# Optimization experiments

Measured on AMD Instinct MI355X. Metric: run time of the kernel, lower is better.

The kernel has to match this reference:

```python
import jax, jax.numpy as jnp
import numpy as np

NH, K = 16, 4  # num_heads, num_points


def _ln(x, g, b):
    m = x.mean(-1, keepdims=True)
    v = jnp.var(x, axis=-1, keepdims=True)
    return (x - m) / jnp.sqrt(v + 1e-5) * g + b


def setup_inputs() -> dict:
    key = jax.random.key(0)
    ks = jax.random.split(key, 12)
    B, S, D = 16, 1024, 1024
    HD = D // NH
    def lin(k, fi, fo, scale=1.0):
        return jax.random.normal(k, (fi, fo), jnp.float32) * (scale / np.sqrt(fi))
    z = lambda n: jnp.zeros((n,), jnp.float32)
    return {
        "source": jax.random.normal(ks[0], (B, S, D), jnp.float32),
        "target": jax.random.normal(ks[1], (B, S, D), jnp.float32),
        "Wq": lin(ks[2], D, D), "bq": z(D),
        "Wo1": lin(ks[3], HD, 64), "bo1": z(64),
        "Wo2": lin(ks[4], 64, 2 * K, 0.1), "bo2": z(2 * K),
        "Wa": lin(ks[5], HD, K), "ba": z(K),
        "Wv": lin(ks[6], D, D), "bv": z(D),
        "Wout": lin(ks[7], D, D), "bout": z(D),
        "gq": jnp.ones((D,), jnp.float32), "bq_ln": z(D),
        "gkv": jnp.ones((D,), jnp.float32), "bkv_ln": z(D),
        "gffn": jnp.ones((D,), jnp.float32), "bffn_ln": z(D),
        "W1": lin(ks[8], D, 4 * D), "b1": z(4 * D),
        "W2": lin(ks[9], 4 * D, D), "b2": z(D),
    }


def _forward(source, target, Wq, bq, Wo1, bo1, Wo2, bo2, Wa, ba, Wv, bv,
             Wout, bout, gq, bq_ln, gkv, bkv_ln, gffn, bffn_ln, W1, b1, W2, b2):
    B, S, D = source.shape
    HD = D // NH
    Hs = int(round(S ** 0.5)); Ws = Hs  # S = H*W square grid

    q_norm = _ln(source, gq, bq_ln)
    v_norm = _ln(target, gkv, bkv_ln)
    q = (q_norm @ Wq + bq).reshape(B, S, NH, HD)
    # value map per head: (B, NH, H, W, HD)
    v = (v_norm @ Wv + bv).reshape(B, Hs, Ws, NH, HD).transpose(0, 3, 1, 2, 4)
    v_flat = v.reshape(B, NH, Hs * Ws, HD)

    # learned offsets: tanh(MLP(q)) * 0.5, in normalized [-1,1] coords
    h = jax.nn.relu(q @ Wo1 + bo1)
    off = jnp.tanh((h @ Wo2 + bo2).reshape(B, S, NH, K, 2)) * 0.5

    # reference grid: ref_grid[i*W+j] = (ref_x[j], ref_y[i])
    rx = jnp.linspace(-1.0, 1.0, Ws)
    ry = jnp.linspace(-1.0, 1.0, Hs)
    gx, gy = jnp.meshgrid(rx, ry)  # 'xy' indexing
    ref = jnp.stack([gx, gy], -1).reshape(S, 2)
    pts = ref[None, :, None, None, :] + off  # (B, S, NH, K, 2), last dim = (x, y)

    # grid_sample, bilinear, align_corners=True, padding_mode='zeros'
    x = (pts[..., 0] + 1.0) * 0.5 * (Ws - 1)
    y = (pts[..., 1] + 1.0) * 0.5 * (Hs - 1)
    x = jnp.moveaxis(x, 1, 2)  # (B, NH, S, K)
    y = jnp.moveaxis(y, 1, 2)
    x0 = jnp.floor(x); y0 = jnp.floor(y)
    wx1 = x - x0; wy1 = y - y0
    x0i = x0.astype(jnp.int32); y0i = y0.astype(jnp.int32)

    def gather(xi, yi, w):
        m = (xi >= 0) & (xi <= Ws - 1) & (yi >= 0) & (yi <= Hs - 1)
        idx = jnp.clip(yi, 0, Hs - 1) * Ws + jnp.clip(xi, 0, Ws - 1)
        g = jnp.take_along_axis(v_flat, idx.reshape(B, NH, S * K, 1), axis=2)
        return g.reshape(B, NH, S, K, HD) * (w * m)[..., None]

    sampled = (gather(x0i, y0i, (1.0 - wx1) * (1.0 - wy1))
               + gather(x0i + 1, y0i, wx1 * (1.0 - wy1))
               + gather(x0i, y0i + 1, (1.0 - wx1) * wy1)
               + gather(x0i + 1, y0i + 1, wx1 * wy1))  # (B, NH, S, K, HD)

    attn = jax.nn.softmax(q @ Wa + ba, axis=-1)  # (B, S, NH, K)
    head_out = jnp.einsum('bsnk,bnskd->bsnd', attn, sampled).reshape(B, S, D)

    src = source + (head_out @ Wout + bout)
    f = jax.nn.gelu(_ln(src, gffn, bffn_ln) @ W1 + b1, approximate=False)
    return src + (f @ W2 + b2)


def reference(source, target, Wq, bq, Wo1, bo1, Wo2, bo2, Wa, ba, Wv, bv,
              Wout, bout, gq, bq_ln, gkv, bkv_ln, gffn, bffn_ln, W1, b1, W2, b2):
    return _forward(source, target, Wq, bq, Wo1, bo1, Wo2, bo2, Wa, ba, Wv, bv,
                    Wout, bout, gq, bq_ln, gkv, bkv_ln, gffn, bffn_ln, W1, b1, W2, b2)
```

## Files before the change

### kernel.cpp

```cpp
#include <hip/hip_runtime.h>

typedef __attribute__((ext_vector_type(8))) short short8;
typedef __attribute__((ext_vector_type(4))) float f32x4;

#define DEV __device__ __forceinline__

DEV float bf2f(unsigned short u) { return __uint_as_float(((unsigned)u) << 16); }
DEV unsigned short f2bf(float f) {
  unsigned u = __float_as_uint(f);
  u += 0x7FFF + ((u >> 16) & 1);
  return (unsigned short)(u >> 16);
}

#define GLOAD_LDS16(gptr, lptr)                                                              \
  __builtin_amdgcn_global_load_lds((const __attribute__((address_space(1))) void*)(gptr),   \
                                   (__attribute__((address_space(3))) void*)(lptr), 16, 0, 0)

__global__ __launch_bounds__(256) void wt_transpose_bf16(const float* __restrict__ W,
                                                         unsigned short* __restrict__ Wt,
                                                         int K, int N) {
  __shared__ float t[32][33];
  int k0 = blockIdx.x * 32, n0 = blockIdx.y * 32;
  int tx = threadIdx.x, ty = threadIdx.y;
#pragma unroll
  for (int i = 0; i < 4; ++i)
    t[ty + 8 * i][tx] = W[(long)(k0 + ty + 8 * i) * N + n0 + tx];
  __syncthreads();
#pragma unroll
  for (int i = 0; i < 4; ++i)
    Wt[(long)(n0 + ty + 8 * i) * K + k0 + tx] = f2bf(t[tx][ty + 8 * i]);
}

__global__ __launch_bounds__(256) void ln_to_bf16(const float* __restrict__ x,
                                                  const float* __restrict__ g,
                                                  const float* __restrict__ b,
                                                  unsigned short* __restrict__ y) {
  const long row = blockIdx.x;
  const int tid = threadIdx.x;
  float4 v = *(const float4*)(x + row * 1024 + tid * 4);
  float s = v.x + v.y + v.z + v.w;
  float s2 = v.x * v.x + v.y * v.y + v.z * v.z + v.w * v.w;
#pragma unroll
  for (int o = 32; o > 0; o >>= 1) { s += __shfl_down(s, o); s2 += __shfl_down(s2, o); }
  __shared__ float red[8];
  __shared__ float mv[2];
  int wv = tid >> 6, ln = tid & 63;
  if (ln == 0) { red[wv] = s; red[4 + wv] = s2; }
  __syncthreads();
  if (tid == 0) {
    float a = red[0] + red[1] + red[2] + red[3];
    float q = red[4] + red[5] + red[6] + red[7];
    float mean = a * (1.f / 1024.f);
    mv[0] = mean;
    mv[1] = rsqrtf(q * (1.f / 1024.f) - mean * mean + 1e-5f);
  }
  __syncthreads();
  float mean = mv[0], rstd = mv[1];
  float4 gg = *(const float4*)(g + tid * 4);
  float4 bb = *(const float4*)(b + tid * 4);
  ushort4 o;
  o.x = f2bf((v.x - mean) * rstd * gg.x + bb.x);
  o.y = f2bf((v.y - mean) * rstd * gg.y + bb.y);
  o.z = f2bf((v.z - mean) * rstd * gg.z + bb.z);
  o.w = f2bf((v.w - mean) * rstd * gg.w + bb.w);
  *(ushort4*)(y + row * 1024 + tid * 4) = o;
}

template <int EPI>
__global__ __launch_bounds__(512, 2) void gemm_bf16(const unsigned short* __restrict__ A,
                                                    const unsigned short* __restrict__ Bt,
                                                    const float* __restrict__ bias,
                                                    const float* __restrict__ res,
                                                    void* __restrict__ out,
                                                    int N, int K, int ldb) {
  __shared__ __align__(16) char smem[131072];
  const int tid = threadIdx.x;
  const int wave = tid >> 6, lane = tid & 63;
  const int wm = wave >> 2, wn = wave & 3;
  const long row0 = (long)blockIdx.x * 256;
  const long col0 = (long)blockIdx.y * 256;
  const int NT = K >> 5;

  f32x4 acc[8][4];
#pragma unroll
  for (int i = 0; i < 8; ++i)
#pragma unroll
    for (int n = 0; n < 4; ++n) acc[i][n] = f32x4{0.f, 0.f, 0.f, 0.f};

  const int srow = wave * 16 + (lane >> 2);
  const int kc_ph = lane & 3;

  auto STAGE = [&](const unsigned short* base, long ld, long r0, int U, char* dst16k) {
#pragma unroll
    for (int j = 0; j < 2; ++j) {
      const int row = j * 128 + srow;
      const int kc = kc_ph ^ ((row >> 1) & 3);
      GLOAD_LDS16(base + (r0 + row) * ld + U * 32 + kc * 8, dst16k + j * 8192 + wave * 1024);
    }
  };
  auto RD = [&](const char* sb, int row) -> short8 {
    const int kc = (lane >> 4) ^ ((row >> 1) & 3);
    return *(const short8*)(sb + row * 64 + kc * 16);
  };

#pragma unroll
  for (int U = 0; U < 3; ++U) {
    STAGE(A, K, row0, U, smem + U * 32768);
    STAGE(Bt, ldb, col0, U, smem + U * 32768 + 16384);
  }
  asm volatile("s_waitcnt vmcnt(8)" ::: "memory");
  __builtin_amdgcn_s_barrier();

  for (int T = 0; T < NT; ++T) {
    const char* sA = smem + (T & 3) * 32768;
    const char* sB = sA + 16384;
    char* stslot = smem + ((T + 3) & 3) * 32768;
    const bool do_stage = (T + 3 < NT);

    short8 af[4], bf[4];
#pragma unroll
    for (int i = 0; i < 4; ++i) af[i] = RD(sA, wm * 128 + i * 16 + (lane & 15));
#pragma unroll
    for (int n = 0; n < 4; ++n) bf[n] = RD(sB, wn * 64 + n * 16 + (lane & 15));
    if (do_stage) STAGE(A, K, row0, T + 3, stslot);
    __builtin_amdgcn_s_barrier();
    __builtin_amdgcn_s_setprio(1);
#pragma unroll
    for (int i = 0; i < 4; ++i)
#pragma unroll
      for (int n = 0; n < 4; ++n)
        acc[i][n] = __builtin_amdgcn_mfma_f32_16x16x32_bf16(af[i], bf[n], acc[i][n], 0, 0, 0);
    __builtin_amdgcn_s_setprio(0);
    __builtin_amdgcn_s_barrier();

#pragma unroll
    for (int i = 0; i < 4; ++i) af[i] = RD(sA, wm * 128 + 64 + i * 16 + (lane & 15));
    if (do_stage) STAGE(Bt, ldb, col0, T + 3, stslot + 16384);
    if (T < NT - 3) {
      asm volatile("s_waitcnt vmcnt(8)" ::: "memory");
    } else if (T == NT - 3) {
      asm volatile("s_waitcnt vmcnt(4)" ::: "memory");
    } else if (T == NT - 2) {
      asm volatile("s_waitcnt vmcnt(0)" ::: "memory");
    }
    __builtin_amdgcn_s_barrier();
    __builtin_amdgcn_s_setprio(1);
#pragma unroll
    for (int i = 0; i < 4; ++i)
#pragma unroll
      for (int n = 0; n < 4; ++n)
        acc[4 + i][n] =
            __builtin_amdgcn_mfma_f32_16x16x32_bf16(af[i], bf[n], acc[4 + i][n], 0, 0, 0);
    __builtin_amdgcn_s_setprio(0);
    __builtin_amdgcn_s_barrier();
  }

  const int lr = lane >> 4, lc = lane & 15;
#pragma unroll
  for (int i = 0; i < 8; ++i) {
#pragma unroll
    for (int n = 0; n < 4; ++n) {
      const long gcol = col0 + wn * 64 + n * 16 + lc;
      const float bvv = (EPI == 5) ? 0.f : bias[gcol];
#pragma unroll
      for (int r = 0; r < 4; ++r) {
        const long grow = row0 + wm * 128 + i * 16 + lr * 4 + r;
        float val = acc[i][n][r] + bvv;
        if (EPI == 0) {
          ((float*)out)[grow * N + gcol] = val;
        } else if (EPI == 1) {
          const int b_ = (int)(grow >> 10), hw = (int)(grow & 1023);
          const int nh = (int)(gcol >> 6), hd = (int)(gcol & 63);
          ((unsigned short*)out)[((long)(b_ * 16 + nh) << 16) + hw * 64 + hd] = f2bf(val);
        } else if (EPI == 2) {
          ((float*)out)[grow * N + gcol] = val + res[grow * N + gcol];
        } else if (EPI == 3) {
          float gl = 0.5f * val * (1.f + erff(val * 0.70710678118654752f));
          ((unsigned short*)out)[grow * N + gcol] = f2bf(gl);
        } else {
          ((float*)out)[grow * N + gcol] = val + res[grow * N + gcol];
        }
      }
    }
  }
}

__global__ __launch_bounds__(256) void offset_attn_mlp(
    const float* __restrict__ qf,
    const float* __restrict__ Wo1, const float* __restrict__ bo1,
    const float* __restrict__ Wo2, const float* __restrict__ bo2,
    const float* __restrict__ Wa, const float* __restrict__ ba,
    float* __restrict__ coords) {
  const int r = blockIdx.x * 256 + threadIdx.x;
  const int s = (r >> 4) & 1023;

  float qr[64];
  const float* qp = qf + (long)r * 64;
#pragma unroll
  for (int i = 0; i < 16; ++i) *(float4*)(qr + 4 * i) = *(const float4*)(qp + 4 * i);

  float off[8];
#pragma unroll
  for (int o = 0; o < 8; ++o) off[o] = bo2[o];

#pragma unroll 1
  for (int jj = 0; jj < 8; ++jj) {
    float hacc[8];
#pragma unroll
    for (int o = 0; o < 8; ++o) hacc[o] = bo1[jj * 8 + o];
#pragma unroll
    for (int i = 0; i < 64; ++i) {
      const float qv = qr[i];
#pragma unroll
      for (int o = 0; o < 8; ++o) hacc[o] = fmaf(qv, Wo1[i * 64 + jj * 8 + o], hacc[o]);
    }
#pragma unroll
    for (int jo = 0; jo < 8; ++jo) {
      const float hj = fmaxf(hacc[jo], 0.f);
      const int j = jj * 8 + jo;
#pragma unroll
      for (int o = 0; o < 8; ++o) off[o] = fmaf(hj, Wo2[j * 8 + o], off[o]);
    }
  }

  float lg[4];
#pragma unroll
  for (int k = 0; k < 4; ++k) lg[k] = ba[k];
#pragma unroll
  for (int i = 0; i < 64; ++i) {
    const float qv = qr[i];
#pragma unroll
    for (int k = 0; k < 4; ++k) lg[k] = fmaf(qv, Wa[i * 4 + k], lg[k]);
  }
  const float mx = fmaxf(fmaxf(lg[0], lg[1]), fmaxf(lg[2], lg[3]));
  const float e0 = expf(lg[0] - mx), e1 = expf(lg[1] - mx), e2 = expf(lg[2] - mx),
              e3 = expf(lg[3] - mx);
  const float inv = 1.f / (e0 + e1 + e2 + e3);

  const float sx = (float)(s & 31), sy = (float)(s >> 5);
  float4 xv, yv, av;
  xv.x = sx + tanhf(off[0]) * 7.75f; yv.x = sy + tanhf(off[1]) * 7.75f;
  xv.y = sx + tanhf(off[2]) * 7.75f; yv.y = sy + tanhf(off[3]) * 7.75f;
  xv.z = sx + tanhf(off[4]) * 7.75f; yv.z = sy + tanhf(off[5]) * 7.75f;
  xv.w = sx + tanhf(off[6]) * 7.75f; yv.w = sy + tanhf(off[7]) * 7.75f;
  av.x = e0 * inv; av.y = e1 * inv; av.z = e2 * inv; av.w = e3 * inv;
  float* cp = coords + (long)r * 16;
  *(float4*)(cp + 0) = xv;
  *(float4*)(cp + 4) = yv;
  *(float4*)(cp + 8) = av;
}

__global__ __launch_bounds__(256) void deform_gather(
    const unsigned short* __restrict__ v_flat, const float* __restrict__ coords,
    unsigned short* __restrict__ head_out) {
  const int tid = threadIdx.x, wave = tid >> 6, lane = tid & 63;
  const int m = blockIdx.x * 4 + wave;
  const int b = m >> 14, nh = (m >> 10) & 15, s = m & 1023;
  const long r = (long)(b * 1024 + s) * 16 + nh;

  float cf = 0.f;
  if (lane < 12) cf = coords[r * 16 + lane];
  const unsigned short* vb = v_flat + ((long)(b * 16 + nh) << 16);

  float o = 0.f;
#pragma unroll
  for (int k = 0; k < 4; ++k) {
    const float xp = __shfl(cf, k), yp = __shfl(cf, 4 + k), ak = __shfl(cf, 8 + k);
    const float x0f = floorf(xp), y0f = floorf(yp);
    const int x0 = (int)x0f, y0 = (int)y0f;
    const float wx1 = xp - x0f, wy1 = yp - y0f;
    const float wx0 = 1.f - wx1, wy0 = 1.f - wy1;
    float smp = 0.f;
#pragma unroll
    for (int cn = 0; cn < 4; ++cn) {
      const int xi = x0 + (cn & 1), yi = y0 + (cn >> 1);
      const float w = (cn & 1 ? wx1 : wx0) * (cn >> 1 ? wy1 : wy0);
      const bool msk = (xi >= 0) & (xi <= 31) & (yi >= 0) & (yi <= 31);
      const int xc = min(max(xi, 0), 31), yc = min(max(yi, 0), 31);
      const float vv = bf2f(vb[(yc * 32 + xc) * 64 + lane]);
      smp = fmaf(vv, msk ? w : 0.f, smp);
    }
    o = fmaf(ak, smp, o);
  }
  head_out[r * 64 + lane] = f2bf(o);
}

extern "C" void kernel_launch(void* const* d_in, const int* in_sizes, int n_in,
                              void* d_out, int out_size, void* d_ws, size_t ws_size,
                              hipStream_t stream) {
  const float* source = (const float*)d_in[0];
  const float* target = (const float*)d_in[1];
  const float* Wq = (const float*)d_in[2];
  const float* bq = (const float*)d_in[3];
  const float* Wo1 = (const float*)d_in[4];
  const float* bo1 = (const float*)d_in[5];
  const float* Wo2 = (const float*)d_in[6];
  const float* bo2 = (const float*)d_in[7];
  const float* Wa = (const float*)d_in[8];
  const float* ba = (const float*)d_in[9];
  const float* Wv = (const float*)d_in[10];
  const float* bv = (const float*)d_in[11];
  const float* Wout = (const float*)d_in[12];
  const float* bout = (const float*)d_in[13];
  const float* gq = (const float*)d_in[14];
  const float* bq_ln = (const float*)d_in[15];
  const float* gkv = (const float*)d_in[16];
  const float* bkv_ln = (const float*)d_in[17];
  const float* gffn = (const float*)d_in[18];
  const float* bffn_ln = (const float*)d_in[19];
  const float* W1 = (const float*)d_in[20];
  const float* b1 = (const float*)d_in[21];
  const float* W2 = (const float*)d_in[22];
  const float* b2 = (const float*)d_in[23];

  char* ws = (char*)d_ws;
  const size_t MB = 1u << 20;
  if (ws_size < 150 * MB) return;

  unsigned short* q_norm = (unsigned short*)(ws + 0);
  unsigned short* v_flat = (unsigned short*)(ws + 0);
  unsigned short* v_norm = (unsigned short*)(ws + 32 * MB);
  float* coords = (float*)(ws + 32 * MB);
  unsigned short* ffn_in = (unsigned short*)(ws + 32 * MB);
  float* qf = (float*)(ws + 64 * MB);
  unsigned short* head_out = (unsigned short*)(ws + 64 * MB);
  unsigned short* f_buf = (unsigned short*)(ws + 64 * MB);
  unsigned short* Wq_t = (unsigned short*)(ws + 128 * MB);
  unsigned short* Wv_t = (unsigned short*)(ws + 130 * MB);
  unsigned short* Wout_t = (unsigned short*)(ws + 132 * MB);
  unsigned short* W1_t = (unsigned short*)(ws + 134 * MB);
  unsigned short* W2_t = (unsigned short*)(ws + 142 * MB);
  float* src = (float*)d_out;

  dim3 tb(32, 8);
  wt_transpose_bf16<<<dim3(32, 32), tb, 0, stream>>>(Wq, Wq_t, 1024, 1024);
  wt_transpose_bf16<<<dim3(32, 32), tb, 0, stream>>>(Wv, Wv_t, 1024, 1024);
  wt_transpose_bf16<<<dim3(32, 32), tb, 0, stream>>>(Wout, Wout_t, 1024, 1024);
  wt_transpose_bf16<<<dim3(32, 128), tb, 0, stream>>>(W1, W1_t, 1024, 4096);
  wt_transpose_bf16<<<dim3(128, 32), tb, 0, stream>>>(W2, W2_t, 4096, 1024);

  ln_to_bf16<<<16384, 256, 0, stream>>>(source, gq, bq_ln, q_norm);
  ln_to_bf16<<<16384, 256, 0, stream>>>(target, gkv, bkv_ln, v_norm);

  gemm_bf16<0><<<dim3(64, 4), 512, 0, stream>>>(q_norm, Wq_t, bq, nullptr, qf, 1024, 1024, 1024);
  gemm_bf16<1><<<dim3(64, 4), 512, 0, stream>>>(v_norm, Wv_t, bv, nullptr, v_flat, 1024, 1024, 1024);

  offset_attn_mlp<<<1024, 256, 0, stream>>>(qf, Wo1, bo1, Wo2, bo2, Wa, ba, coords);
  deform_gather<<<65536, 256, 0, stream>>>(v_flat, coords, head_out);

  gemm_bf16<2><<<dim3(64, 4), 512, 0, stream>>>(head_out, Wout_t, bout, source, src, 1024, 1024, 1024);

  ln_to_bf16<<<16384, 256, 0, stream>>>(src, gffn, bffn_ln, ffn_in);

  gemm_bf16<3><<<dim3(64, 8), 512, 0, stream>>>(ffn_in, W1_t, b1, nullptr, f_buf, 2048, 1024, 1024);
  gemm_bf16<2><<<dim3(64, 4), 512, 0, stream>>>(f_buf, W2_t, b2, src, src, 1024, 2048, 4096);
  gemm_bf16<3><<<dim3(64, 8), 512, 0, stream>>>(ffn_in, W1_t + (long)2048 * 1024, b1 + 2048,
                                                nullptr, f_buf, 2048, 1024, 1024);
  gemm_bf16<5><<<dim3(64, 4), 512, 0, stream>>>(f_buf, W2_t + 2048, nullptr, src, src, 1024, 2048, 4096);
}
```

Measured before the change: 873.2 us.

## Replace deep-pipelined 256x256 GEMM with simple 128x128 tile kernel for most GEMMs

The general GEMM now uses 128x128 tiles with 256 threads, a 64-wide K step, an XOR-swizzled 32KB LDS buffer and a full wait plus barrier every iteration, in place of the 4-stage pipelined 256x256 design. A copy of the old deep-pipelined kernel, renamed gemm_deep_gelu, is kept for the first W1 half and now issues its LDS-direct loads through inline asm that sets m0. The goal is more blocks and better occupancy and wave coverage across CUs. The cost is losing load/compute overlap and reading each operand more times from global memory in the simpler kernel.

```diff
diff --git a/kernel.cpp b/kernel.cpp
--- a/kernel.cpp
+++ b/kernel.cpp
@@ -15,6 +15,12 @@
 #define GLOAD_LDS16(gptr, lptr)                                                              \
   __builtin_amdgcn_global_load_lds((const __attribute__((address_space(1))) void*)(gptr),   \
                                    (__attribute__((address_space(3))) void*)(lptr), 16, 0, 0)
+
+DEV void stage16_asm(const void* gaddr, unsigned lds_off_sgpr) {
+  asm volatile("s_mov_b32 m0, %1\n\t"
+               "global_load_lds_dwordx4 %0, off"
+               :: "v"(gaddr), "s"(lds_off_sgpr) : "memory");
+}
 
 __global__ __launch_bounds__(256) void wt_transpose_bf16(const float* __restrict__ W,
                                                          unsigned short* __restrict__ Wt,
@@ -67,105 +73,70 @@
 }
 
 template <int EPI>
-__global__ __launch_bounds__(512, 2) void gemm_bf16(const unsigned short* __restrict__ A,
-                                                    const unsigned short* __restrict__ Bt,
-                                                    const float* __restrict__ bias,
-                                                    const float* __restrict__ res,
-                                                    void* __restrict__ out,
-                                                    int N, int K, int ldb) {
-  __shared__ __align__(16) char smem[131072];
+__global__ __launch_bounds__(256) void gemm_bf16(const unsigned short* __restrict__ A,
+                                                 const unsigned short* __restrict__ Bt,
+                                                 const float* __restrict__ bias,
+                                                 const float* __restrict__ res,
+                                                 void* __restrict__ out,
+                                                 int N, int K, int ldb) {
+  __shared__ __align__(16) char smem[32768];
   const int tid = threadIdx.x;
   const int wave = tid >> 6, lane = tid & 63;
-  const int wm = wave >> 2, wn = wave & 3;
-  const long row0 = (long)blockIdx.x * 256;
-  const long col0 = (long)blockIdx.y * 256;
-  const int NT = K >> 5;
-
-  f32x4 acc[8][4];
-#pragma unroll
-  for (int i = 0; i < 8; ++i)
-#pragma unroll
-    for (int n = 0; n < 4; ++n) acc[i][n] = f32x4{0.f, 0.f, 0.f, 0.f};
-
-  const int srow = wave * 16 + (lane >> 2);
-  const int kc_ph = lane & 3;
-
-  auto STAGE = [&](const unsigned short* base, long ld, long r0, int U, char* dst16k) {
-#pragma unroll
-    for (int j = 0; j < 2; ++j) {
-      const int row = j * 128 + srow;
-      const int kc = kc_ph ^ ((row >> 1) & 3);
-      GLOAD_LDS16(base + (r0 + row) * ld + U * 32 + kc * 8, dst16k + j * 8192 + wave * 1024);
-    }
-  };
-  auto RD = [&](const char* sb, int row) -> short8 {
-    const int kc = (lane >> 4) ^ ((row >> 1) & 3);
-    return *(const short8*)(sb + row * 64 + kc * 16);
-  };
-
-#pragma unroll
-  for (int U = 0; U < 3; ++U) {
-    STAGE(A, K, row0, U, smem + U * 32768);
-    STAGE(Bt, ldb, col0, U, smem + U * 32768 + 16384);
-  }
-  asm volatile("s_waitcnt vmcnt(8)" ::: "memory");
-  __builtin_amdgcn_s_barrier();
-
-  for (int T = 0; T < NT; ++T) {
-    const char* sA = smem + (T & 3) * 32768;
-    const char* sB = sA + 16384;
-    char* stslot = smem + ((T + 3) & 3) * 32768;
-    const bool do_stage = (T + 3 < NT);
-
-    short8 af[4], bf[4];
-#pragma unroll
-    for (int i = 0; i < 4; ++i) af[i] = RD(sA, wm * 128 + i * 16 + (lane & 15));
-#pragma unroll
-    for (int n = 0; n < 4; ++n) bf[n] = RD(sB, wn * 64 + n * 16 + (lane & 15));
-    if (do_stage) STAGE(A, K, row0, T + 3, stslot);
-    __builtin_amdgcn_s_barrier();
-    __builtin_amdgcn_s_setprio(1);
-#pragma unroll
-    for (int i = 0; i < 4; ++i)
-#pragma unroll
-      for (int n = 0; n < 4; ++n)
-        acc[i][n] = __builtin_amdgcn_mfma_f32_16x16x32_bf16(af[i], bf[n], acc[i][n], 0, 0, 0);
-    __builtin_amdgcn_s_setprio(0);
-    __builtin_amdgcn_s_barrier();
-
-#pragma unroll
-    for (int i = 0; i < 4; ++i) af[i] = RD(sA, wm * 128 + 64 + i * 16 + (lane & 15));
-    if (do_stage) STAGE(Bt, ldb, col0, T + 3, stslot + 16384);
-    if (T < NT - 3) {
-      asm volatile("s_waitcnt vmcnt(8)" ::: "memory");
-    } else if (T == NT - 3) {
-      asm volatile("s_waitcnt vmcnt(4)" ::: "memory");
-    } else if (T == NT - 2) {
-      asm volatile("s_waitcnt vmcnt(0)" ::: "memory");
-    }
-    __builtin_amdgcn_s_barrier();
-    __builtin_amdgcn_s_setprio(1);
-#pragma unroll
-    for (int i = 0; i < 4; ++i)
-#pragma unroll
-      for (int n = 0; n < 4; ++n)
-        acc[4 + i][n] =
-            __builtin_amdgcn_mfma_f32_16x16x32_bf16(af[i], bf[n], acc[4 + i][n], 0, 0, 0);
-    __builtin_amdgcn_s_setprio(0);
-    __builtin_amdgcn_s_barrier();
+  const int wm = wave >> 1, wn = wave & 1;
+  const long row0 = (long)blockIdx.x * 128;
+  const long col0 = (long)blockIdx.y * 128;
+
+  f32x4 acc[4][4];
+#pragma unroll
+  for (int i = 0; i < 4; ++i)
+#pragma unroll
+    for (int j = 0; j < 4; ++j) acc[i][j] = f32x4{0.f, 0.f, 0.f, 0.f};
+
+  const int gg = lane & 7;
+  const int rsub = lane >> 3;
+
+  for (int kt = 0; kt < K; kt += 64) {
+#pragma unroll
+    for (int i = 0; i < 4; ++i) {
+      const int c = wave * 4 + i;
+      const int r = c * 8 + rsub;
+      const int kg = gg ^ rsub;
+      GLOAD_LDS16(A + (row0 + r) * (long)K + kt + kg * 8, smem + c * 1024);
+      GLOAD_LDS16(Bt + (col0 + r) * (long)ldb + kt + kg * 8, smem + 16384 + c * 1024);
+    }
+    asm volatile("s_waitcnt vmcnt(0)" ::: "memory");
+    __syncthreads();
+#pragma unroll
+    for (int ks = 0; ks < 2; ++ks) {
+      short8 af[4], bfr[4];
+#pragma unroll
+      for (int i = 0; i < 4; ++i) {
+        const int rowa = wm * 64 + i * 16 + (lane & 15);
+        const int rowb = wn * 64 + i * 16 + (lane & 15);
+        const int kb = ks * 64 + (lane >> 4) * 16;
+        af[i] = *(const short8*)(smem + rowa * 128 + (kb ^ ((rowa & 7) << 4)));
+        bfr[i] = *(const short8*)(smem + 16384 + rowb * 128 + (kb ^ ((rowb & 7) << 4)));
+      }
+#pragma unroll
+      for (int i = 0; i < 4; ++i)
+#pragma unroll
+        for (int j = 0; j < 4; ++j)
+          acc[i][j] = __builtin_amdgcn_mfma_f32_16x16x32_bf16(af[i], bfr[j], acc[i][j], 0, 0, 0);
+    }
+    __syncthreads();
   }
 
   const int lr = lane >> 4, lc = lane & 15;
 #pragma unroll
-  for (int i = 0; i < 8; ++i) {
-#pragma unroll
-    for (int n = 0; n < 4; ++n) {
-      const long gcol = col0 + wn * 64 + n * 16 + lc;
+  for (int i = 0; i < 4; ++i) {
+#pragma unroll
+    for (int j = 0; j < 4; ++j) {
+      const long gcol = col0 + wn * 64 + j * 16 + lc;
       const float bvv = (EPI == 5) ? 0.f : bias[gcol];
 #pragma unroll
       for (int r = 0; r < 4; ++r) {
-        const long grow = row0 + wm * 128 + i * 16 + lr * 4 + r;
-        float val = acc[i][n][r] + bvv;
+        const long grow = row0 + wm * 64 + i * 16 + lr * 4 + r;
+        float val = acc[i][j][r] + bvv;
         if (EPI == 0) {
           ((float*)out)[grow * N + gcol] = val;
         } else if (EPI == 1) {
@@ -180,6 +151,115 @@
         } else {
           ((float*)out)[grow * N + gcol] = val + res[grow * N + gcol];
         }
+      }
+    }
+  }
+}
+
+__global__ __launch_bounds__(512, 2) void gemm_deep_gelu(const unsigned short* __restrict__ A,
+                                                         const unsigned short* __restrict__ Bt,
+                                                         const float* __restrict__ bias,
+                                                         unsigned short* __restrict__ out,
+                                                         int N, int K, int ldb) {
+  __shared__ __align__(16) char smem[131072];
+  const int tid = threadIdx.x;
+  const int wave = tid >> 6, lane = tid & 63;
+  const int wm = wave >> 2, wn = wave & 3;
+  const long row0 = (long)blockIdx.x * 256;
+  const long col0 = (long)blockIdx.y * 256;
+  const int NT = K >> 5;
+  const unsigned lds0 =
+      (unsigned)(size_t)(__attribute__((address_space(3))) char*)smem;
+
+  f32x4 acc[8][4];
+#pragma unroll
+  for (int i = 0; i < 8; ++i)
+#pragma unroll
+    for (int n = 0; n < 4; ++n) acc[i][n] = f32x4{0.f, 0.f, 0.f, 0.f};
+
+  const int srow = wave * 16 + (lane >> 2);
+  const int kc_ph = lane & 3;
+
+  auto STAGE = [&](const unsigned short* base, long ld, long r0, int U, unsigned dst16k) {
+#pragma unroll
+    for (int j = 0; j < 2; ++j) {
+      const int row = j * 128 + srow;
+      const int kc = kc_ph ^ ((row >> 1) & 3);
+      const unsigned lo =
+          __builtin_amdgcn_readfirstlane(dst16k + (unsigned)(j * 8192 + wave * 1024));
+      stage16_asm(base + (r0 + row) * ld + U * 32 + kc * 8, lo);
+    }
+  };
+  auto RD = [&](const char* sb, int row) -> short8 {
+    const int kc = (lane >> 4) ^ ((row >> 1) & 3);
+    return *(const short8*)(sb + row * 64 + kc * 16);
+  };
+
+#pragma unroll
+  for (int U = 0; U < 3; ++U) {
+    STAGE(A, K, row0, U, lds0 + U * 32768);
+    STAGE(Bt, ldb, col0, U, lds0 + U * 32768 + 16384);
+  }
+  asm volatile("s_waitcnt vmcnt(8)" ::: "memory");
+  __builtin_amdgcn_s_barrier();
+
+  for (int T = 0; T < NT; ++T) {
+    const char* sA = smem + (T & 3) * 32768;
+    const char* sB = sA + 16384;
+    const unsigned stslot = lds0 + ((T + 3) & 3) * 32768;
+    const bool do_stage = (T + 3 < NT);
+
+    short8 af[4], bf[4];
+#pragma unroll
+    for (int i = 0; i < 4; ++i) af[i] = RD(sA, wm * 128 + i * 16 + (lane & 15));
+#pragma unroll
+    for (int n = 0; n < 4; ++n) bf[n] = RD(sB, wn * 64 + n * 16 + (lane & 15));
+    if (do_stage) STAGE(A, K, row0, T + 3, stslot);
+    __builtin_amdgcn_s_barrier();
+    __builtin_amdgcn_s_setprio(1);
+#pragma unroll
+    for (int i = 0; i < 4; ++i)
+#pragma unroll
+      for (int n = 0; n < 4; ++n)
+        acc[i][n] = __builtin_amdgcn_mfma_f32_16x16x32_bf16(af[i], bf[n], acc[i][n], 0, 0, 0);
+    __builtin_amdgcn_s_setprio(0);
+    __builtin_amdgcn_s_barrier();
+
+#pragma unroll
+    for (int i = 0; i < 4; ++i) af[i] = RD(sA, wm * 128 + 64 + i * 16 + (lane & 15));
+    if (do_stage) STAGE(Bt, ldb, col0, T + 3, stslot + 16384);
+    if (T < NT - 3) {
+      asm volatile("s_waitcnt vmcnt(8)" ::: "memory");
+    } else if (T == NT - 3) {
+      asm volatile("s_waitcnt vmcnt(4)" ::: "memory");
+    } else if (T == NT - 2) {
+      asm volatile("s_waitcnt vmcnt(0)" ::: "memory");
+    }
+    __builtin_amdgcn_s_barrier();
+    __builtin_amdgcn_s_setprio(1);
+#pragma unroll
+    for (int i = 0; i < 4; ++i)
+#pragma unroll
+      for (int n = 0; n < 4; ++n)
+        acc[4 + i][n] =
+            __builtin_amdgcn_mfma_f32_16x16x32_bf16(af[i], bf[n], acc[4 + i][n], 0, 0, 0);
+    __builtin_amdgcn_s_setprio(0);
+    __builtin_amdgcn_s_barrier();
+  }
+
+  const int lr = lane >> 4, lc = lane & 15;
+#pragma unroll
+  for (int i = 0; i < 8; ++i) {
+#pragma unroll
+    for (int n = 0; n < 4; ++n) {
+      const long gcol = col0 + wn * 64 + n * 16 + lc;
+      const float bvv = bias[gcol];
+#pragma unroll
+      for (int r = 0; r < 4; ++r) {
+        const long grow = row0 + wm * 128 + i * 16 + lr * 4 + r;
+        float val = acc[i][n][r] + bvv;
+        float gl = 0.5f * val * (1.f + erff(val * 0.70710678118654752f));
+        out[grow * N + gcol] = f2bf(gl);
       }
     }
   }
@@ -342,19 +422,19 @@
   ln_to_bf16<<<16384, 256, 0, stream>>>(source, gq, bq_ln, q_norm);
   ln_to_bf16<<<16384, 256, 0, stream>>>(target, gkv, bkv_ln, v_norm);
 
-  gemm_bf16<0><<<dim3(64, 4), 512, 0, stream>>>(q_norm, Wq_t, bq, nullptr, qf, 1024, 1024, 1024);
-  gemm_bf16<1><<<dim3(64, 4), 512, 0, stream>>>(v_norm, Wv_t, bv, nullptr, v_flat, 1024, 1024, 1024);
+  gemm_bf16<0><<<dim3(128, 8), 256, 0, stream>>>(q_norm, Wq_t, bq, nullptr, qf, 1024, 1024, 1024);
+  gemm_bf16<1><<<dim3(128, 8), 256, 0, stream>>>(v_norm, Wv_t, bv, nullptr, v_flat, 1024, 1024, 1024);
 
   offset_attn_mlp<<<1024, 256, 0, stream>>>(qf, Wo1, bo1, Wo2, bo2, Wa, ba, coords);
   deform_gather<<<65536, 256, 0, stream>>>(v_flat, coords, head_out);
 
-  gemm_bf16<2><<<dim3(64, 4), 512, 0, stream>>>(head_out, Wout_t, bout, source, src, 1024, 1024, 1024);
+  gemm_bf16<2><<<dim3(128, 8), 256, 0, stream>>>(head_out, Wout_t, bout, source, src, 1024, 1024, 1024);
 
   ln_to_bf16<<<16384, 256, 0, stream>>>(src, gffn, bffn_ln, ffn_in);
 
-  gemm_bf16<3><<<dim3(64, 8), 512, 0, stream>>>(ffn_in, W1_t, b1, nullptr, f_buf, 2048, 1024, 1024);
-  gemm_bf16<2><<<dim3(64, 4), 512, 0, stream>>>(f_buf, W2_t, b2, src, src, 1024, 2048, 4096);
-  gemm_bf16<3><<<dim3(64, 8), 512, 0, stream>>>(ffn_in, W1_t + (long)2048 * 1024, b1 + 2048,
-                                                nullptr, f_buf, 2048, 1024, 1024);
-  gemm_bf16<5><<<dim3(64, 4), 512, 0, stream>>>(f_buf, W2_t + 2048, nullptr, src, src, 1024, 2048, 4096);
-}
+  gemm_deep_gelu<<<dim3(64, 8), 512, 0, stream>>>(ffn_in, W1_t, b1, f_buf, 2048, 1024, 1024);
+  gemm_bf16<2><<<dim3(128, 8), 256, 0, stream>>>(f_buf, W2_t, b2, src, src, 1024, 2048, 4096);
+  gemm_bf16<3><<<dim3(128, 16), 256, 0, stream>>>(ffn_in, W1_t + (long)2048 * 1024, b1 + 2048,
+                                                  nullptr, f_buf, 2048, 1024, 1024);
+  gemm_bf16<5><<<dim3(128, 8), 256, 0, stream>>>(f_buf, W2_t + 2048, nullptr, src, src, 1024, 2048, 4096);
+}
```

Result: slower. 1.077 ms (+23.3%).
